# Kernel tuning notes

Measured on AMD Instinct MI355X. Metric: run time of the kernel, lower is better.

## Reference

```python
import jax, jax.numpy as jnp
import numpy as np

B, N = 8, 2048
DIN, DS, DO, GE, HID = 2, 32, 32, 8, 32
CHEB_K = 3
N_SUPPORTS = 2
D_CAT = DIN + 2 * DS            # 66, input to the two AGCNs
D_BASIS = N_SUPPORTS * CHEB_K * D_CAT  # 396


def setup_inputs() -> dict:
    key = jax.random.key(0)
    ks = jax.random.split(key, 12)
    xt = jax.random.normal(ks[0], (B, N, DIN), dtype=jnp.float32)
    state1 = jax.random.normal(ks[1], (B, N, DS), dtype=jnp.float32)
    state2 = jax.random.normal(ks[2], (B, N, DS), dtype=jnp.float32)
    gatembedding = jax.random.normal(ks[3], (B, N, GE), dtype=jnp.float32)
    # adaptive adjacency supports: row-stochastic (softmax over neighbors), 2 supports
    supports = jax.nn.softmax(jax.random.normal(ks[4], (N_SUPPORTS, B, N, N), dtype=jnp.float32), axis=-1)

    def xavier(k, shape):
        fan_in, fan_out = shape[0], shape[1]
        std = float(np.sqrt(2.0 / (fan_in + fan_out)))
        return jax.random.normal(k, shape, dtype=jnp.float32) * std

    return {
        "xt": xt, "state1": state1, "state2": state2,
        "gatembedding": gatembedding, "supports": supports,
        "mlp_w": xavier(ks[5], (DIN + 2 * DS + GE, DO)), "mlp_b": jnp.zeros((DO,), jnp.float32),
        "gate_w": xavier(ks[6], (D_BASIS, 3 * DO)), "gate_b": jnp.zeros((3 * DO,), jnp.float32),
        "upd_w": xavier(ks[7], (D_BASIS, DO)), "upd_b": jnp.zeros((DO,), jnp.float32),
        "hop_w": xavier(ks[8], (DO, HID)), "hop_b": jnp.zeros((HID,), jnp.float32),
    }


def _agcn(x, supports, W, b):
    """Chebyshev graph conv: for each support, basis T0=I, T1=A, Tk=2A Tk-1 - Tk-2,
    applied to x (linearity lets us recurse on T_k @ x directly, same math)."""
    terms = []
    for i in range(N_SUPPORTS):  # fixed small structural loop
        A = supports[i]                                  # [B,N,N]
        t_prev, t_cur = x, jnp.einsum('bnm,bmc->bnc', A, x)
        ts = [t_prev, t_cur]
        for _ in range(2, CHEB_K):
            t_prev, t_cur = t_cur, 2.0 * jnp.einsum('bnm,bmc->bnc', A, t_cur) - t_prev
            ts.append(t_cur)
        terms.extend(ts)
    x_g = jnp.concatenate(terms, axis=-1)                # [B,N,2*K*c]
    return jnp.einsum('bni,io->bno', x_g, W) + b


def reference(xt, state1, state2, gatembedding, supports,
              mlp_w, mlp_b, gate_w, gate_b, upd_w, upd_b, hop_w, hop_b):
    # MLP mixing gate between the two incoming states
    gate_in = jnp.concatenate([xt, state1, state2, gatembedding], axis=-1)
    mr = jax.nn.sigmoid(gate_in @ mlp_w + mlp_b)
    state = mr * state1 + (1.0 - mr) * state2
    # graph-conv GRU gates
    X = jnp.concatenate([xt, state1, state2], axis=-1)   # [B,N,DIN+2*DS]
    zz_r = jax.nn.sigmoid(_agcn(X, supports, gate_w, gate_b))
    z1, z2, r = zz_r[..., :DO], zz_r[..., DO:2 * DO], zz_r[..., 2 * DO:]
    candidate = jnp.concatenate([xt, z1 * state1, z2 * state2], axis=-1)
    hc = jnp.tanh(_agcn(candidate, supports, upd_w, upd_b))
    h = r * state + (1.0 - r) * hc                        # [B,N,DO]
    transnext = h @ hop_w + hop_b                         # [B,N,HID]
    return (h, transnext)
```

## Files before the change

### kernel.cpp

```cpp
#include <hip/hip_runtime.h>

#define NN 2048
#define BB 8
#define KT 416
#define SLOT (80 * NN)

typedef __bf16 bf16;
typedef __bf16 bf16x4 __attribute__((ext_vector_type(4)));
typedef __bf16 bf16x8 __attribute__((ext_vector_type(8)));
typedef float  f32x4  __attribute__((ext_vector_type(4)));

__global__ void prep_weights(const float* __restrict__ gw, const float* __restrict__ uw,
                             bf16* __restrict__ Wg, bf16* __restrict__ Wu)
{
    int i = blockIdx.x * 256 + threadIdx.x;
    if (i < 96 * KT) {
        int o = i / KT, k = i % KT, t = k / 80, c = k % 80;
        float v = 0.0f;
        if (c < 66) {
            if (t == 0)      v = gw[c*96+o] - gw[(132+c)*96+o] + gw[(198+c)*96+o] - gw[(330+c)*96+o];
            else if (t == 1) v = gw[(66+c)*96+o];
            else if (t == 2) v = 2.0f * gw[(132+c)*96+o];
            else if (t == 3) v = gw[(264+c)*96+o];
            else             v = 2.0f * gw[(330+c)*96+o];
        }
        Wg[i] = (bf16)v;
    }
    if (i < 32 * KT) {
        int o = i / KT, k = i % KT, t = k / 80, c = k % 80;
        float v = 0.0f;
        if (c < 66) {
            if (t == 0)      v = uw[c*32+o] - uw[(132+c)*32+o] + uw[(198+c)*32+o] - uw[(330+c)*32+o];
            else if (t == 1) v = uw[(66+c)*32+o];
            else if (t == 2) v = 2.0f * uw[(132+c)*32+o];
            else if (t == 3) v = uw[(264+c)*32+o];
            else             v = 2.0f * uw[(330+c)*32+o];
        }
        Wu[i] = (bf16)v;
    }
}

__global__ __launch_bounds__(256)
void prep_nodes(const float* __restrict__ xt, const float* __restrict__ s1,
                const float* __restrict__ s2, const float* __restrict__ ge,
                const float* __restrict__ mlp_w, const float* __restrict__ mlp_b,
                float* __restrict__ state, bf16* __restrict__ T)
{
    __shared__ float wl[74 * 32];
    __shared__ float bl[32];
    __shared__ __align__(16) float statel[64][36];
    __shared__ __align__(16) bf16  Xl[80][72];
    const int tid = threadIdx.x;

    for (int i = tid; i < 592; i += 256) ((float4*)wl)[i] = ((const float4*)mlp_w)[i];
    if (tid < 32) bl[tid] = mlp_b[tid];
    {
        int bb = blockIdx.x >> 5, chunk = blockIdx.x & 31;
        uint2* dst = (uint2*)((char*)T + ((size_t)bb * KT * NN + 400 * NN) * 2 + (size_t)chunk * 2048);
        dst[tid] = make_uint2(0u, 0u);
    }
    for (int i = tid; i < 14 * 64; i += 256) Xl[66 + (i >> 6)][i & 63] = (bf16)0.0f;
    __syncthreads();

    const int nl = tid & 63, og = tid >> 6, o0 = og * 8;
    const size_t node0 = (size_t)blockIdx.x * 64;
    const size_t node = node0 + nl;
    const int b = (int)(node0 >> 11);
    const int nb0 = (int)(node0 & 2047);
    const float* p1 = s1 + node * 32;
    const float* p2 = s2 + node * 32;
    const float* pg = ge + node * 8;

    float acc[8];
    #pragma unroll
    for (int j = 0; j < 8; ++j) acc[j] = bl[o0 + j];
    float2 px = *(const float2*)(xt + node * 2);
    #pragma unroll
    for (int j = 0; j < 8; ++j) acc[j] += px.x * wl[o0 + j] + px.y * wl[32 + o0 + j];

    float k1[8], k2[8];
    #pragma unroll
    for (int ii = 0; ii < 8; ++ii) {
        float4 v = *(const float4*)(p1 + ii * 4);
        const float* vp = (const float*)&v;
        if (ii == 2 * og)     { k1[0]=vp[0]; k1[1]=vp[1]; k1[2]=vp[2]; k1[3]=vp[3]; }
        if (ii == 2 * og + 1) { k1[4]=vp[0]; k1[5]=vp[1]; k1[6]=vp[2]; k1[7]=vp[3]; }
        #pragma unroll
        for (int p = 0; p < 4; ++p) {
            #pragma unroll
            for (int j = 0; j < 8; ++j) acc[j] += vp[p] * wl[(2 + ii*4 + p) * 32 + o0 + j];
        }
    }
    #pragma unroll
    for (int ii = 0; ii < 8; ++ii) {
        float4 v = *(const float4*)(p2 + ii * 4);
        const float* vp = (const float*)&v;
        if (ii == 2 * og)     { k2[0]=vp[0]; k2[1]=vp[1]; k2[2]=vp[2]; k2[3]=vp[3]; }
        if (ii == 2 * og + 1) { k2[4]=vp[0]; k2[5]=vp[1]; k2[6]=vp[2]; k2[7]=vp[3]; }
        #pragma unroll
        for (int p = 0; p < 4; ++p) {
            #pragma unroll
            for (int j = 0; j < 8; ++j) acc[j] += vp[p] * wl[(34 + ii*4 + p) * 32 + o0 + j];
        }
    }
    #pragma unroll
    for (int ii = 0; ii < 2; ++ii) {
        float4 v = *(const float4*)(pg + ii * 4);
        const float* vp = (const float*)&v;
        #pragma unroll
        for (int p = 0; p < 4; ++p) {
            #pragma unroll
            for (int j = 0; j < 8; ++j) acc[j] += vp[p] * wl[(66 + ii*4 + p) * 32 + o0 + j];
        }
    }
    #pragma unroll
    for (int j = 0; j < 8; ++j) {
        float mr = 1.0f / (1.0f + __expf(-acc[j]));
        statel[nl][o0 + j] = mr * k1[j] + (1.0f - mr) * k2[j];
        Xl[2 + o0 + j][nl]  = (bf16)k1[j];
        Xl[34 + o0 + j][nl] = (bf16)k2[j];
    }
    if (og == 0) { Xl[0][nl] = (bf16)px.x; Xl[1][nl] = (bf16)px.y; }
    __syncthreads();

    for (int i = tid; i < 512; i += 256) {
        int n_ = i >> 3, c = (i & 7) * 4;
        *(float4*)&state[node0 * 32 + n_ * 32 + c] = *(const float4*)&statel[n_][c];
    }
    bf16* Tb = T + (size_t)b * KT * NN;
    for (int i = tid; i < 640; i += 256) {
        int r = i >> 3, seg = i & 7;
        *(uint4*)(Tb + (size_t)r * NN + nb0 + seg * 8) = *(const uint4*)&Xl[r][seg * 8];
    }
}

template<int MODE>
__global__ __launch_bounds__(256, 2)
void gemm_cheb(const float* __restrict__ Aall, bf16* Abf, bf16* T,
               int in0, int in1, int out0, int out1)
{
    __shared__ __align__(16) bf16 lA[2][64][40];
    __shared__ __align__(16) bf16 lB[2][80][40];

    const int sb = blockIdx.y;
    const int s = sb >> 3, b = sb & 7;
    const int m0 = blockIdx.x * 64;
    const float* A = Aall + (size_t)sb * NN * NN + (size_t)m0 * NN;
    bf16* Ab = Abf + (size_t)sb * NN * NN + (size_t)m0 * NN;
    bf16* Tb = T + (size_t)b * KT * NN;
    const bf16* Bt = Tb + (size_t)(s ? in1 : in0) * SLOT;
    bf16*       Ct = Tb + (size_t)(s ? out1 : out0) * SLOT + m0;

    const int tid  = threadIdx.x;
    const int wave = tid >> 6;
    const int lane = tid & 63;

    const int arow = tid >> 3, aseg = tid & 7;
    const int arw2 = tid >> 2, asg2 = tid & 3;
    const int brow = tid >> 2, bseg = tid & 3;
    const int brow2 = 64 + (tid >> 2);

    float4 ra0, ra1; uint4 ra2; uint4 rb0, rb1;

    auto gload = [&](int k0) {
        if constexpr (MODE == 2) {
            ra2 = *(const uint4*)(Ab + (size_t)arw2 * NN + k0 + asg2 * 8);
        } else {
            ra0 = *(const float4*)(A + (size_t)arow * NN + k0 + aseg * 4);
            ra1 = *(const float4*)(A + (size_t)(arow + 32) * NN + k0 + aseg * 4);
        }
        rb0 = *(const uint4*)(Bt + (size_t)brow * NN + k0 + bseg * 8);
        if (tid < 64) rb1 = *(const uint4*)(Bt + (size_t)brow2 * NN + k0 + bseg * 8);
    };
    auto stage = [&](int buf, int k0) {
        if constexpr (MODE == 2) {
            *(uint4*)&lA[buf][arw2][asg2 * 8] = ra2;
        } else {
            bf16x4 a0, a1;
            a0[0]=(bf16)ra0.x; a0[1]=(bf16)ra0.y; a0[2]=(bf16)ra0.z; a0[3]=(bf16)ra0.w;
            a1[0]=(bf16)ra1.x; a1[1]=(bf16)ra1.y; a1[2]=(bf16)ra1.z; a1[3]=(bf16)ra1.w;
            *(bf16x4*)&lA[buf][arow][aseg * 4]      = a0;
            *(bf16x4*)&lA[buf][arow + 32][aseg * 4] = a1;
            if constexpr (MODE == 1) {
                *(bf16x4*)(Ab + (size_t)arow * NN + k0 + aseg * 4)        = a0;
                *(bf16x4*)(Ab + (size_t)(arow + 32) * NN + k0 + aseg * 4) = a1;
            }
        }
        *(uint4*)&lB[buf][brow][bseg * 8] = rb0;
        if (tid < 64) *(uint4*)&lB[buf][brow2][bseg * 8] = rb1;
    };

    f32x4 acc[5] = {};
    const int frow = lane & 15;
    const int fko  = (lane >> 4) * 8;

    gload(0);
    #pragma unroll 2
    for (int kt = 0; kt < 64; ++kt) {
        const int buf = kt & 1;
        stage(buf, kt * 32);
        if (kt < 63) gload((kt + 1) * 32);
        __syncthreads();
        bf16x8 af = *(const bf16x8*)&lA[buf][wave * 16 + frow][fko];
        #pragma unroll
        for (int ct = 0; ct < 5; ++ct) {
            bf16x8 bv = *(const bf16x8*)&lB[buf][ct * 16 + frow][fko];
            acc[ct] = __builtin_amdgcn_mfma_f32_16x16x32_bf16(af, bv, acc[ct], 0, 0, 0);
        }
    }

    const int ccol = lane & 15;
    const int crow = (lane >> 4) * 4;
    #pragma unroll
    for (int ct = 0; ct < 5; ++ct) {
        bf16x4 o;
        o[0]=(bf16)acc[ct][0]; o[1]=(bf16)acc[ct][1]; o[2]=(bf16)acc[ct][2]; o[3]=(bf16)acc[ct][3];
        *(bf16x4*)&Ct[(size_t)(ct * 16 + ccol) * NN + wave * 16 + crow] = o;
    }
}

__global__ __launch_bounds__(256)
void proj_gate(const bf16* T, const bf16* __restrict__ Wg, const float* __restrict__ gate_b,
               const float* __restrict__ s1, const float* __restrict__ s2,
               bf16* Tmut, float* __restrict__ rT)
{
    __shared__ __align__(16) bf16 Wl[96][424];
    __shared__ __align__(16) bf16 Bl[2][64][44];
    const int b = blockIdx.y, n0 = blockIdx.x * 64, tid = threadIdx.x;
    const bf16* Tb = T + (size_t)b * KT * NN;

    for (int i = tid; i < 96 * 52; i += 256) {
        int r = i / 52, seg = i % 52;
        *(uint4*)&Wl[r][seg * 8] = *(const uint4*)(Wg + (size_t)r * KT + seg * 8);
    }
    const int kk = tid >> 3, seg = tid & 7;
    uint4 rb;
    auto gload = [&](int k0) { rb = *(const uint4*)(Tb + (size_t)(k0 + kk) * NN + n0 + seg * 8); };
    auto scat = [&](int buf) {
        bf16 tmp[8]; *(uint4*)tmp = rb;
        #pragma unroll
        for (int j = 0; j < 8; ++j) Bl[buf][seg * 8 + j][kk] = tmp[j];
    };
    const int lane = tid & 63, wave = tid >> 6;
    const int fr = lane & 15, qd = lane >> 4;

    f32x4 acc[6] = {};
    gload(0);
    for (int st = 0; st < 13; ++st) {
        const int buf = st & 1;
        scat(buf);
        if (st < 12) gload((st + 1) * 32);
        __syncthreads();
        bf16x8 bv = *(const bf16x8*)&Bl[buf][wave * 16 + fr][qd * 8];
        #pragma unroll
        for (int f = 0; f < 6; ++f) {
            bf16x8 av = *(const bf16x8*)&Wl[f * 16 + fr][st * 32 + qd * 8];
            acc[f] = __builtin_amdgcn_mfma_f32_16x16x32_bf16(av, bv, acc[f], 0, 0, 0);
        }
    }

    const int nn = n0 + wave * 16 + fr;
    const size_t node = (size_t)b * NN + nn;
    bf16* Cd = Tmut + (size_t)b * KT * NN;
    #pragma unroll
    for (int f = 0; f < 6; ++f) {
        const int o0 = f * 16 + qd * 4;
        float4 gb4 = *(const float4*)(gate_b + o0);
        const float* gb = (const float*)&gb4;
        float sg[4];
        #pragma unroll
        for (int r = 0; r < 4; ++r) sg[r] = 1.0f / (1.0f + __expf(-(acc[f][r] + gb[r])));
        if (f < 2) {
            float4 sv4 = *(const float4*)(s1 + node * 32 + o0);
            const float* sv = (const float*)&sv4;
            #pragma unroll
            for (int r = 0; r < 4; ++r) Cd[(size_t)(2 + o0 + r) * NN + nn] = (bf16)(sg[r] * sv[r]);
        } else if (f < 4) {
            const int oo = o0 - 32;
            float4 sv4 = *(const float4*)(s2 + node * 32 + oo);
            const float* sv = (const float*)&sv4;
            #pragma unroll
            for (int r = 0; r < 4; ++r) Cd[(size_t)(34 + oo + r) * NN + nn] = (bf16)(sg[r] * sv[r]);
        } else {
            const int oo = o0 - 64;
            #pragma unroll
            for (int r = 0; r < 4; ++r) rT[((size_t)b * 32 + oo + r) * NN + nn] = sg[r];
        }
    }
}

__global__ __launch_bounds__(256)
void proj_upd(const bf16* __restrict__ T, const bf16* __restrict__ Wu,
              const float* __restrict__ upd_b, const float* __restrict__ state,
              const float* __restrict__ rT, const float* __restrict__ hop_w,
              const float* __restrict__ hop_b, float* __restrict__ out)
{
    __shared__ __align__(16) bf16 Wl[32][424];
    __shared__ __align__(16) bf16 Bl[2][64][44];
    __shared__ __align__(16) float hsh[64][36];
    __shared__ float hw[1024];
    const int b = blockIdx.y, n0 = blockIdx.x * 64, tid = threadIdx.x;
    const bf16* Tb = T + (size_t)b * KT * NN;

    for (int i = tid; i < 32 * 52; i += 256) {
        int r = i / 52, seg = i % 52;
        *(uint4*)&Wl[r][seg * 8] = *(const uint4*)(Wu + (size_t)r * KT + seg * 8);
    }
    for (int i = tid; i < 256; i += 256) ((float4*)hw)[i] = ((const float4*)hop_w)[i];
    const int kk = tid >> 3, seg = tid & 7;
    uint4 rb;
    auto gload = [&](int k0) { rb = *(const uint4*)(Tb + (size_t)(k0 + kk) * NN + n0 + seg * 8); };
    auto scat = [&](int buf) {
        bf16 tmp[8]; *(uint4*)tmp = rb;
        #pragma unroll
        for (int j = 0; j < 8; ++j) Bl[buf][seg * 8 + j][kk] = tmp[j];
    };
    const int lane = tid & 63, wave = tid >> 6;
    const int fr = lane & 15, qd = lane >> 4;

    f32x4 acc[2] = {};
    gload(0);
    for (int st = 0; st < 13; ++st) {
        const int buf = st & 1;
        scat(buf);
        if (st < 12) gload((st + 1) * 32);
        __syncthreads();
        bf16x8 bv = *(const bf16x8*)&Bl[buf][wave * 16 + fr][qd * 8];
        #pragma unroll
        for (int f = 0; f < 2; ++f) {
            bf16x8 av = *(const bf16x8*)&Wl[f * 16 + fr][st * 32 + qd * 8];
            acc[f] = __builtin_amdgcn_mfma_f32_16x16x32_bf16(av, bv, acc[f], 0, 0, 0);
        }
    }

    const int nn = n0 + wave * 16 + fr;
    const size_t node = (size_t)b * NN + nn;
    const int nl = wave * 16 + fr;
    #pragma unroll
    for (int f = 0; f < 2; ++f) {
        const int o0 = f * 16 + qd * 4;
        float4 ub4 = *(const float4*)(upd_b + o0);
        const float* ub = (const float*)&ub4;
        float4 st4 = *(const float4*)(state + node * 32 + o0);
        const float* sv = (const float*)&st4;
        #pragma unroll
        for (int r = 0; r < 4; ++r) {
            const int o = o0 + r;
            float hc = tanhf(acc[f][r] + ub[r]);
            float rv = rT[((size_t)b * 32 + o) * NN + nn];
            hsh[nl][o] = rv * sv[r] + (1.0f - rv) * hc;
        }
    }
    __syncthreads();

    const int nl2 = tid & 63, og = tid >> 6;
    const size_t node2 = (size_t)b * NN + n0 + nl2;
    float tac[8];
    #pragma unroll
    for (int j = 0; j < 8; ++j) tac[j] = hop_b[og * 8 + j];
    #pragma unroll
    for (int kc = 0; kc < 8; ++kc) {
        float4 hv4 = *(const float4*)&hsh[nl2][kc * 4];
        const float* hv = (const float*)&hv4;
        #pragma unroll
        for (int p = 0; p < 4; ++p) {
            #pragma unroll
            for (int j = 0; j < 8; ++j) tac[j] += hv[p] * hw[(kc * 4 + p) * 32 + og * 8 + j];
        }
    }
    float* out2 = out + (size_t)BB * NN * 32;
    *(float4*)&out[node2 * 32 + og * 8]     = *(const float4*)&hsh[nl2][og * 8];
    *(float4*)&out[node2 * 32 + og * 8 + 4] = *(const float4*)&hsh[nl2][og * 8 + 4];
    float4 t0; float* t0p = (float*)&t0;
    t0p[0]=tac[0]; t0p[1]=tac[1]; t0p[2]=tac[2]; t0p[3]=tac[3];
    *(float4*)&out2[node2 * 32 + og * 8] = t0;
    t0p[0]=tac[4]; t0p[1]=tac[5]; t0p[2]=tac[6]; t0p[3]=tac[7];
    *(float4*)&out2[node2 * 32 + og * 8 + 4] = t0;
}

extern "C" void kernel_launch(void* const* d_in, const int* in_sizes, int n_in,
                              void* d_out, int out_size, void* d_ws, size_t ws_size,
                              hipStream_t stream)
{
    const float* xt     = (const float*)d_in[0];
    const float* s1     = (const float*)d_in[1];
    const float* s2     = (const float*)d_in[2];
    const float* ge     = (const float*)d_in[3];
    const float* sup    = (const float*)d_in[4];
    const float* mlp_w  = (const float*)d_in[5];
    const float* mlp_b  = (const float*)d_in[6];
    const float* gate_w = (const float*)d_in[7];
    const float* gate_b = (const float*)d_in[8];
    const float* upd_w  = (const float*)d_in[9];
    const float* upd_b  = (const float*)d_in[10];
    const float* hop_w  = (const float*)d_in[11];
    const float* hop_b  = (const float*)d_in[12];
    float* out = (float*)d_out;

    char* ws = (char*)d_ws;
    size_t off = 0;
    auto alloc = [&](size_t bytes) -> void* {
        void* p = ws + off;
        off += (bytes + 255) & ~(size_t)255;
        return p;
    };
    bf16*  T     = (bf16*) alloc((size_t)BB * KT * NN * 2);
    float* state = (float*)alloc((size_t)BB * NN * 32 * 4);
    float* rT    = (float*)alloc((size_t)BB * 32 * NN * 4);
    bf16*  Wg    = (bf16*) alloc((size_t)96 * KT * 2);
    bf16*  Wu    = (bf16*) alloc((size_t)32 * KT * 2);
    bf16*  Abf   = (bf16*) (ws + off);
    const bool useA = (off + (size_t)16 * NN * NN * 2) <= ws_size;

    prep_weights<<<156, 256, 0, stream>>>(gate_w, upd_w, Wg, Wu);
    prep_nodes<<<256, 256, 0, stream>>>(xt, s1, s2, ge, mlp_w, mlp_b, state, T);

    if (useA) {
        gemm_cheb<1><<<dim3(32, 16), 256, 0, stream>>>(sup, Abf, T, 0, 0, 1, 3);
        gemm_cheb<2><<<dim3(32, 16), 256, 0, stream>>>(sup, Abf, T, 1, 3, 2, 4);
        proj_gate<<<dim3(32, 8), 256, 0, stream>>>(T, Wg, gate_b, s1, s2, T, rT);
        gemm_cheb<2><<<dim3(32, 16), 256, 0, stream>>>(sup, Abf, T, 0, 0, 1, 3);
        gemm_cheb<2><<<dim3(32, 16), 256, 0, stream>>>(sup, Abf, T, 1, 3, 2, 4);
    } else {
        gemm_cheb<0><<<dim3(32, 16), 256, 0, stream>>>(sup, Abf, T, 0, 0, 1, 3);
        gemm_cheb<0><<<dim3(32, 16), 256, 0, stream>>>(sup, Abf, T, 1, 3, 2, 4);
        proj_gate<<<dim3(32, 8), 256, 0, stream>>>(T, Wg, gate_b, s1, s2, T, rT);
        gemm_cheb<0><<<dim3(32, 16), 256, 0, stream>>>(sup, Abf, T, 0, 0, 1, 3);
        gemm_cheb<0><<<dim3(32, 16), 256, 0, stream>>>(sup, Abf, T, 1, 3, 2, 4);
    }
    proj_upd<<<dim3(32, 8), 256, 0, stream>>>(T, Wu, upd_b, state, rT, hop_w, hop_b, out);
}
```

Baseline: 584.9 us.

## Split-K the Chebyshev GEMMs into two halves with a separate reduction kernel

Each graph-conv GEMM now splits the 2048-long K dimension across two blocks (grid z=2), doubling the block count from 512 to 1024 so more of the GPU is busy. Each split writes fp32 partials to a new workspace buffer, and a new reduce_split kernel sums the two partials and writes bf16 into the T buffer. The main loop also becomes a manually double-buffered register/LDS pipeline, and launch bounds are raised to 4 blocks per SM. The cost is extra global traffic for fp32 partials, four extra kernel launches, and higher register pressure.

```diff
diff --git a/kernel.cpp b/kernel.cpp
--- a/kernel.cpp
+++ b/kernel.cpp
@@ -134,10 +134,12 @@
     }
 }
 
+struct Q { float4 a0, a1; uint4 a2, b0, b1; };
+
 template<int MODE>
-__global__ __launch_bounds__(256, 2)
-void gemm_cheb(const float* __restrict__ Aall, bf16* Abf, bf16* T,
-               int in0, int in1, int out0, int out1)
+__global__ __launch_bounds__(256, 4)
+void gemm_cheb(const float* __restrict__ Aall, bf16* Abf, const bf16* __restrict__ T,
+               float* __restrict__ P, int in0, int in1)
 {
     __shared__ __align__(16) bf16 lA[2][64][40];
     __shared__ __align__(16) bf16 lB[2][80][40];
@@ -145,11 +147,11 @@
     const int sb = blockIdx.y;
     const int s = sb >> 3, b = sb & 7;
     const int m0 = blockIdx.x * 64;
+    const int kb = blockIdx.z * 1024;
     const float* A = Aall + (size_t)sb * NN * NN + (size_t)m0 * NN;
     bf16* Ab = Abf + (size_t)sb * NN * NN + (size_t)m0 * NN;
-    bf16* Tb = T + (size_t)b * KT * NN;
-    const bf16* Bt = Tb + (size_t)(s ? in1 : in0) * SLOT;
-    bf16*       Ct = Tb + (size_t)(s ? out1 : out0) * SLOT + m0;
+    const bf16* Bt = T + (size_t)b * KT * NN + (size_t)(s ? in1 : in0) * SLOT;
+    float* Pd = P + ((size_t)blockIdx.z * 16 + sb) * (size_t)SLOT + m0;
 
     const int tid  = threadIdx.x;
     const int wave = tid >> 6;
@@ -160,25 +162,25 @@
     const int brow = tid >> 2, bseg = tid & 3;
     const int brow2 = 64 + (tid >> 2);
 
-    float4 ra0, ra1; uint4 ra2; uint4 rb0, rb1;
-
-    auto gload = [&](int k0) {
+    Q qA, qB;
+
+    auto gload = [&](Q& q, int k0) {
         if constexpr (MODE == 2) {
-            ra2 = *(const uint4*)(Ab + (size_t)arw2 * NN + k0 + asg2 * 8);
+            q.a2 = *(const uint4*)(Ab + (size_t)arw2 * NN + k0 + asg2 * 8);
         } else {
-            ra0 = *(const float4*)(A + (size_t)arow * NN + k0 + aseg * 4);
-            ra1 = *(const float4*)(A + (size_t)(arow + 32) * NN + k0 + aseg * 4);
-        }
-        rb0 = *(const uint4*)(Bt + (size_t)brow * NN + k0 + bseg * 8);
-        if (tid < 64) rb1 = *(const uint4*)(Bt + (size_t)brow2 * NN + k0 + bseg * 8);
-    };
-    auto stage = [&](int buf, int k0) {
+            q.a0 = *(const float4*)(A + (size_t)arow * NN + k0 + aseg * 4);
+            q.a1 = *(const float4*)(A + (size_t)(arow + 32) * NN + k0 + aseg * 4);
+        }
+        q.b0 = *(const uint4*)(Bt + (size_t)brow * NN + k0 + bseg * 8);
+        if (tid < 64) q.b1 = *(const uint4*)(Bt + (size_t)brow2 * NN + k0 + bseg * 8);
+    };
+    auto stage = [&](Q& q, int buf, int k0) {
         if constexpr (MODE == 2) {
-            *(uint4*)&lA[buf][arw2][asg2 * 8] = ra2;
+            *(uint4*)&lA[buf][arw2][asg2 * 8] = q.a2;
         } else {
             bf16x4 a0, a1;
-            a0[0]=(bf16)ra0.x; a0[1]=(bf16)ra0.y; a0[2]=(bf16)ra0.z; a0[3]=(bf16)ra0.w;
-            a1[0]=(bf16)ra1.x; a1[1]=(bf16)ra1.y; a1[2]=(bf16)ra1.z; a1[3]=(bf16)ra1.w;
+            a0[0]=(bf16)q.a0.x; a0[1]=(bf16)q.a0.y; a0[2]=(bf16)q.a0.z; a0[3]=(bf16)q.a0.w;
+            a1[0]=(bf16)q.a1.x; a1[1]=(bf16)q.a1.y; a1[2]=(bf16)q.a1.z; a1[3]=(bf16)q.a1.w;
             *(bf16x4*)&lA[buf][arow][aseg * 4]      = a0;
             *(bf16x4*)&lA[buf][arow + 32][aseg * 4] = a1;
             if constexpr (MODE == 1) {
@@ -186,37 +188,62 @@
                 *(bf16x4*)(Ab + (size_t)(arow + 32) * NN + k0 + aseg * 4) = a1;
             }
         }
-        *(uint4*)&lB[buf][brow][bseg * 8] = rb0;
-        if (tid < 64) *(uint4*)&lB[buf][brow2][bseg * 8] = rb1;
+        *(uint4*)&lB[buf][brow][bseg * 8] = q.b0;
+        if (tid < 64) *(uint4*)&lB[buf][brow2][bseg * 8] = q.b1;
     };
 
     f32x4 acc[5] = {};
     const int frow = lane & 15;
     const int fko  = (lane >> 4) * 8;
 
-    gload(0);
-    #pragma unroll 2
-    for (int kt = 0; kt < 64; ++kt) {
-        const int buf = kt & 1;
-        stage(buf, kt * 32);
-        if (kt < 63) gload((kt + 1) * 32);
-        __syncthreads();
+    auto compute = [&](int buf) {
         bf16x8 af = *(const bf16x8*)&lA[buf][wave * 16 + frow][fko];
         #pragma unroll
         for (int ct = 0; ct < 5; ++ct) {
             bf16x8 bv = *(const bf16x8*)&lB[buf][ct * 16 + frow][fko];
             acc[ct] = __builtin_amdgcn_mfma_f32_16x16x32_bf16(af, bv, acc[ct], 0, 0, 0);
         }
+    };
+
+    gload(qA, kb);
+    gload(qB, kb + 32);
+
+    #pragma unroll 1
+    for (int kt = 0; kt < 32; kt += 2) {
+        stage(qA, 0, kb + kt * 32);
+        if (kt + 2 < 32) gload(qA, kb + (kt + 2) * 32);
+        __syncthreads();
+        compute(0);
+        stage(qB, 1, kb + (kt + 1) * 32);
+        if (kt + 3 < 32) gload(qB, kb + (kt + 3) * 32);
+        __syncthreads();
+        compute(1);
     }
 
     const int ccol = lane & 15;
     const int crow = (lane >> 4) * 4;
     #pragma unroll
     for (int ct = 0; ct < 5; ++ct) {
-        bf16x4 o;
-        o[0]=(bf16)acc[ct][0]; o[1]=(bf16)acc[ct][1]; o[2]=(bf16)acc[ct][2]; o[3]=(bf16)acc[ct][3];
-        *(bf16x4*)&Ct[(size_t)(ct * 16 + ccol) * NN + wave * 16 + crow] = o;
-    }
+        *(f32x4*)&Pd[(size_t)(ct * 16 + ccol) * NN + wave * 16 + crow] = acc[ct];
+    }
+}
+
+__global__ __launch_bounds__(256)
+void reduce_split(const float* __restrict__ P, bf16* __restrict__ T, int out0, int out1)
+{
+    const int sb = blockIdx.y;
+    const int j = blockIdx.x * 256 + threadIdx.x;
+    const int row = j >> 9, col = (j & 511) * 4;
+    const float* p0 = P + (size_t)sb * SLOT + (size_t)row * NN + col;
+    const float* p1 = p0 + (size_t)16 * SLOT;
+    float4 v0 = *(const float4*)p0;
+    float4 v1 = *(const float4*)p1;
+    bf16x4 o;
+    o[0] = (bf16)(v0.x + v1.x); o[1] = (bf16)(v0.y + v1.y);
+    o[2] = (bf16)(v0.z + v1.z); o[3] = (bf16)(v0.w + v1.w);
+    bf16* dst = T + (size_t)(sb & 7) * KT * NN
+                  + (size_t)((sb >> 3) ? out1 : out0) * SLOT + (size_t)row * NN + col;
+    *(bf16x4*)dst = o;
 }
 
 __global__ __launch_bounds__(256)
@@ -409,24 +436,34 @@
     float* rT    = (float*)alloc((size_t)BB * 32 * NN * 4);
     bf16*  Wg    = (bf16*) alloc((size_t)96 * KT * 2);
     bf16*  Wu    = (bf16*) alloc((size_t)32 * KT * 2);
+    float* P     = (float*)alloc((size_t)2 * 16 * SLOT * 4);
     bf16*  Abf   = (bf16*) (ws + off);
     const bool useA = (off + (size_t)16 * NN * NN * 2) <= ws_size;
 
     prep_weights<<<156, 256, 0, stream>>>(gate_w, upd_w, Wg, Wu);
     prep_nodes<<<256, 256, 0, stream>>>(xt, s1, s2, ge, mlp_w, mlp_b, state, T);
 
+    const dim3 gg(32, 16, 2), gr(160, 16);
     if (useA) {
-        gemm_cheb<1><<<dim3(32, 16), 256, 0, stream>>>(sup, Abf, T, 0, 0, 1, 3);
-        gemm_cheb<2><<<dim3(32, 16), 256, 0, stream>>>(sup, Abf, T, 1, 3, 2, 4);
+        gemm_cheb<1><<<gg, 256, 0, stream>>>(sup, Abf, T, P, 0, 0);
+        reduce_split<<<gr, 256, 0, stream>>>(P, T, 1, 3);
+        gemm_cheb<2><<<gg, 256, 0, stream>>>(sup, Abf, T, P, 1, 3);
+        reduce_split<<<gr, 256, 0, stream>>>(P, T, 2, 4);
         proj_gate<<<dim3(32, 8), 256, 0, stream>>>(T, Wg, gate_b, s1, s2, T, rT);
-        gemm_cheb<2><<<dim3(32, 16), 256, 0, stream>>>(sup, Abf, T, 0, 0, 1, 3);
-        gemm_cheb<2><<<dim3(32, 16), 256, 0, stream>>>(sup, Abf, T, 1, 3, 2, 4);
+        gemm_cheb<2><<<gg, 256, 0, stream>>>(sup, Abf, T, P, 0, 0);
+        reduce_split<<<gr, 256, 0, stream>>>(P, T, 1, 3);
+        gemm_cheb<2><<<gg, 256, 0, stream>>>(sup, Abf, T, P, 1, 3);
+        reduce_split<<<gr, 256, 0, stream>>>(P, T, 2, 4);
     } else {
-        gemm_cheb<0><<<dim3(32, 16), 256, 0, stream>>>(sup, Abf, T, 0, 0, 1, 3);
-        gemm_cheb<0><<<dim3(32, 16), 256, 0, stream>>>(sup, Abf, T, 1, 3, 2, 4);
+        gemm_cheb<0><<<gg, 256, 0, stream>>>(sup, Abf, T, P, 0, 0);
+        reduce_split<<<gr, 256, 0, stream>>>(P, T, 1, 3);
+        gemm_cheb<0><<<gg, 256, 0, stream>>>(sup, Abf, T, P, 1, 3);
+        reduce_split<<<gr, 256, 0, stream>>>(P, T, 2, 4);
         proj_gate<<<dim3(32, 8), 256, 0, stream>>>(T, Wg, gate_b, s1, s2, T, rT);
-        gemm_cheb<0><<<dim3(32, 16), 256, 0, stream>>>(sup, Abf, T, 0, 0, 1, 3);
-        gemm_cheb<0><<<dim3(32, 16), 256, 0, stream>>>(sup, Abf, T, 1, 3, 2, 4);
+        gemm_cheb<0><<<gg, 256, 0, stream>>>(sup, Abf, T, P, 0, 0);
+        reduce_split<<<gr, 256, 0, stream>>>(P, T, 1, 3);
+        gemm_cheb<0><<<gg, 256, 0, stream>>>(sup, Abf, T, P, 1, 3);
+        reduce_split<<<gr, 256, 0, stream>>>(P, T, 2, 4);
     }
     proj_upd<<<dim3(32, 8), 256, 0, stream>>>(T, Wu, upd_b, state, rT, hop_w, hop_b, out);
 }
```

Result: slower. 868.6 us (+48.5%).
